# Optimization experiments

Hardware: AMD Instinct MI355X
Metric: run time of the kernel (lower is better)

## Reference

```python
import jax, jax.numpy as jnp
import numpy as np

B, T, N, E, I, H = 8, 168, 425, 2048, 128, 256
F1, F2 = 10, 32  # GCN hidden dims


def gcn(x, src, dst, w, W, b):
    """PyG-style GCNConv on one graph: x [N,f_in], src/dst [E], w [E]."""
    n = x.shape[0]
    h = x @ W  # [N, f_out]
    sl = jnp.arange(n, dtype=src.dtype)  # self loops, weight 1
    s = jnp.concatenate([src, sl])
    d = jnp.concatenate([dst, sl])
    ww = jnp.concatenate([w, jnp.ones((n,), w.dtype)])
    deg = jax.ops.segment_sum(ww, d, num_segments=n)
    dinv = jnp.where(deg > 0, jax.lax.rsqrt(jnp.maximum(deg, 1e-12)), 0.0)
    norm = dinv[s] * ww * dinv[d]
    return jax.ops.segment_sum(norm[:, None] * h[s], d, num_segments=n) + b


# vectorize over (batch, time)
_gcn_bt = jax.vmap(jax.vmap(gcn, in_axes=(0, 0, 0, 0, None, None)),
                   in_axes=(0, 0, 0, 0, None, None))


def lstm(xs, h0, c0, Wih, Whh, bih, bhh):
    """Single-layer torch LSTM (gate order i,f,g,o). xs [B,T,I] -> [B,T,H]."""
    def step(carry, x):
        h, c = carry
        g = x @ Wih.T + h @ Whh.T + bih + bhh  # [B,4H]
        i, f, gg, o = jnp.split(g, 4, axis=-1)
        c = jax.nn.sigmoid(f) * c + jax.nn.sigmoid(i) * jnp.tanh(gg)
        h = jax.nn.sigmoid(o) * jnp.tanh(c)
        return (h, c), h
    _, ys = jax.lax.scan(step, (h0, c0), xs.transpose(1, 0, 2))
    return ys.transpose(1, 0, 2)


def setup_inputs() -> dict:
    key = jax.random.key(0)
    ks = jax.random.split(key, 40)
    def p(i, shape, s=0.05):
        return jax.random.normal(ks[i], shape, jnp.float32) * s
    return {
        "node_feat": jax.random.uniform(ks[0], (B, T, N), jnp.float32),
        "edge_src": jax.random.randint(ks[1], (B, T, E), 0, N, jnp.int32),
        "edge_dst": jax.random.randint(ks[2], (B, T, E), 0, N, jnp.int32),
        "edge_weight": jax.random.uniform(ks[3], (B, T, E), jnp.float32),
        "infect": p(4, (B, T, 25), 1.0),
        "temp": p(5, (B, T, 13), 1.0),
        "h0": p(6, (1, B, H), 1.0),
        "c0": p(7, (1, B, H), 1.0),
        "Wg1": p(8, (1, F1)), "bg1": p(9, (F1,)),
        "Wg2": p(10, (F1, F2)), "bg2": p(11, (F2,)),
        "Wgfc": p(12, (N * F2, I)), "bgfc": p(13, (I,)),
        "Wi1": p(14, (25, 128)), "bi1": p(15, (128,)),
        "Wi2": p(16, (128, 128)), "bi2": p(17, (128,)),
        "Wi3": p(18, (128, 64)), "bi3": p(19, (64,)),
        "Wi4": p(20, (64, I)), "bi4": p(21, (I,)),
        "Wt1": p(22, (13, 64)), "bt1": p(23, (64,)),
        "Wt2": p(24, (64, I)), "bt2": p(25, (I,)),
        "Wcat": p(26, (3 * I, I)), "bcat": p(27, (I,)),
        "Wih": p(28, (4 * H, I)), "Whh": p(29, (4 * H, H)),
        "bih": p(30, (4 * H,)), "bhh": p(31, (4 * H,)),
        "Wfc": p(32, (H, 2 * N)), "bfc": p(33, (2 * N,)),
    }


def reference(node_feat, edge_src, edge_dst, edge_weight, infect, temp, h0, c0,
              Wg1, bg1, Wg2, bg2, Wgfc, bgfc,
              Wi1, bi1, Wi2, bi2, Wi3, bi3, Wi4, bi4,
              Wt1, bt1, Wt2, bt2, Wcat, bcat,
              Wih, Whh, bih, bhh, Wfc, bfc):
    r = jax.nn.relu
    # two-layer GCN per (batch, timestep) graph (deep_graph path)
    x1 = r(_gcn_bt(node_feat[..., None], edge_src, edge_dst, edge_weight, Wg1, bg1))
    x2 = r(_gcn_bt(x1, edge_src, edge_dst, edge_weight, Wg2, bg2))
    g = r(x2.reshape(B, T, N * F2) @ Wgfc + bgfc)  # graph branch [B,T,I]
    inf = r(infect @ Wi1 + bi1)
    inf = r(inf @ Wi2 + bi2)
    inf = r(inf @ Wi3 + bi3)
    inf = r(inf @ Wi4 + bi4)  # infect branch [B,T,I]
    tp = r(temp @ Wt1 + bt1)
    tp = r(tp @ Wt2 + bt2)  # temp branch [B,T,I]
    li = r(jnp.concatenate([g, inf, tp], axis=-1) @ Wcat + bcat)  # concat_fc path
    ys = r(lstm(li, h0[0], c0[0], Wih, Whh, bih, bhh))  # [B,T,H]
    out = r(ys[:, -1] @ Wfc + bfc)  # [B, 2N]
    # original splits by flattening the whole [B,2N] tensor
    flat = out.reshape(-1)
    user_pred = flat[: N * B].reshape(B, N)
    infect_pred = flat[N * B:].reshape(B, N)
    return user_pred, infect_pred
```

## Files before the change

### kernel.cpp

```cpp
#include <hip/hip_runtime.h>
#include <hip/hip_bf16.h>

#define BB 8
#define TT 168
#define NN 425
#define EE 2048
#define II 128
#define HH 256
#define F1 10
#define F2 32
#define BT (BB*TT)
#define K2 (NN*F2)
#define N2 (2*NN)

#define BREG_PW 46
#define BLDS_PW 18
#define BREG_N (8*BREG_PW*64)
#define BLDS_N (8*BLDS_PW*64)
#define LB 2

#define FR_TOTAL 444

typedef _Float16 h2 __attribute__((ext_vector_type(2)));
typedef _Float16 h8 __attribute__((ext_vector_type(8)));
typedef short bf16x8 __attribute__((ext_vector_type(8)));
typedef float f32x4 __attribute__((ext_vector_type(4)));

__device__ __forceinline__ float relu_(float x){ return fmaxf(x, 0.f); }
__device__ __forceinline__ float sigmoid_(float x){ return 1.f/(1.f + expf(-x)); }

#define MFMA16(ACC, AV, BV) \
    ACC = __builtin_amdgcn_mfma_f32_16x16x32_f16((AV), (BV), (ACC), 0, 0, 0)

__device__ __forceinline__ void ds_pk_add(h2* p, h2 v){
    unsigned a = (unsigned)(uintptr_t)p;
    asm volatile("ds_pk_add_f16 %0, %1" :: "v"(a), "v"(v) : "memory");
}

__device__ __forceinline__ h8 actld(const char* act, int K, int lane, int kc){
    int row = lane & 15;
    unsigned off = ((unsigned)(row*K + kc*32 + ((lane>>4)<<3))*2) ^ (unsigned)((row&7)<<4);
    return *(const h8*)(act + off);
}
__device__ __forceinline__ void actst(char* act, int K, int row, int col, _Float16 v){
    unsigned off = ((unsigned)(row*K + col)*2) ^ (unsigned)((row&7)<<4);
    *(_Float16*)(act + off) = v;
}

__global__ __launch_bounds__(256) void gcn_kernel(
    const float* __restrict__ nf, const int* __restrict__ esrc,
    const int* __restrict__ edst, const float* __restrict__ ew,
    const float* __restrict__ Wg1, const float* __restrict__ bg1,
    const float* __restrict__ Wg2, const float* __restrict__ bg2,
    __hip_bfloat16* __restrict__ x2g)
{
    __shared__ float xs[NN];
    __shared__ float dinv[NN];
    __shared__ float agg1[NN];
    __shared__ float nrm[EE];
    __shared__ __align__(16) float x1p[NN*12];
    __shared__ __align__(16) h2 agg2h[NN*8];
    __shared__ float wg1s[F1], bg1s[F1], wg2s[F1*F2], bg2s[F2];

    const int bt = blockIdx.x, tid = threadIdx.x;
    const long eb = (long)bt * EE;

    for (int v = tid; v < NN; v += 256) {
        xs[v] = nf[(long)bt*NN + v];
        dinv[v] = 1.0f;
        agg1[v] = 0.f;
    }
    for (int i = tid; i < NN*8; i += 256) agg2h[i] = (h2){(_Float16)0.f, (_Float16)0.f};
    if (tid < F1) { wg1s[tid] = Wg1[tid]; bg1s[tid] = bg1[tid]; }
    if (tid < F2) bg2s[tid] = bg2[tid];
    for (int i = tid; i < F1*F2; i += 256) wg2s[i] = Wg2[i];
    __syncthreads();

    for (int e = tid; e < EE; e += 256)
        atomicAdd(&dinv[edst[eb+e]], ew[eb+e]);
    __syncthreads();
    for (int v = tid; v < NN; v += 256) {
        float dg = dinv[v];
        dinv[v] = dg > 0.f ? 1.0f / sqrtf(fmaxf(dg, 1e-12f)) : 0.f;
    }
    __syncthreads();

    for (int e = tid; e < EE; e += 256) {
        int s = esrc[eb+e], d = edst[eb+e];
        float nm = dinv[s] * ew[eb+e] * dinv[d];
        nrm[e] = nm;
        atomicAdd(&agg1[d], nm * xs[s]);
    }
    __syncthreads();
    for (int v = tid; v < NN; v += 256) agg1[v] += dinv[v]*dinv[v]*xs[v];
    __syncthreads();
    for (int i = tid; i < NN*12; i += 256) {
        int v = i / 12, f = i - v*12;
        x1p[i] = (f < F1) ? relu_(agg1[v]*wg1s[f] + bg1s[f]) : 0.f;
    }
    __syncthreads();

    for (int e = tid; e < EE; e += 256) {
        int s = esrc[eb+e], d = edst[eb+e];
        float nm = nrm[e];
        float4 a0 = *(const float4*)&x1p[s*12];
        float4 a1 = *(const float4*)&x1p[s*12+4];
        float2 a2 = *(const float2*)&x1p[s*12+8];
        h2 p0; p0[0] = (_Float16)(nm*a0.x); p0[1] = (_Float16)(nm*a0.y);
        h2 p1; p1[0] = (_Float16)(nm*a0.z); p1[1] = (_Float16)(nm*a0.w);
        h2 p2; p2[0] = (_Float16)(nm*a1.x); p2[1] = (_Float16)(nm*a1.y);
        h2 p3; p3[0] = (_Float16)(nm*a1.z); p3[1] = (_Float16)(nm*a1.w);
        h2 p4; p4[0] = (_Float16)(nm*a2.x); p4[1] = (_Float16)(nm*a2.y);
        ds_pk_add(&agg2h[d*8+0], p0);
        ds_pk_add(&agg2h[d*8+1], p1);
        ds_pk_add(&agg2h[d*8+2], p2);
        ds_pk_add(&agg2h[d*8+3], p3);
        ds_pk_add(&agg2h[d*8+4], p4);
    }
    __syncthreads();

    {
        const int k = tid & 31;
        float wk[F1];
        #pragma unroll
        for (int f = 0; f < F1; ++f) wk[f] = wg2s[f*F2 + k];
        for (int i = tid; i < NN*F2; i += 256) {
            int v = i >> 5;
            float dv2 = dinv[v]*dinv[v];
            h8 r8 = *(const h8*)&agg2h[v*8];
            h2 r2 = agg2h[v*8+4];
            float4 a0 = *(const float4*)&x1p[v*12];
            float4 a1 = *(const float4*)&x1p[v*12+4];
            float2 a2 = *(const float2*)&x1p[v*12+8];
            float af[10];
            af[0]=(float)r8[0]+dv2*a0.x; af[1]=(float)r8[1]+dv2*a0.y;
            af[2]=(float)r8[2]+dv2*a0.z; af[3]=(float)r8[3]+dv2*a0.w;
            af[4]=(float)r8[4]+dv2*a1.x; af[5]=(float)r8[5]+dv2*a1.y;
            af[6]=(float)r8[6]+dv2*a1.z; af[7]=(float)r8[7]+dv2*a1.w;
            af[8]=(float)r2[0]+dv2*a2.x; af[9]=(float)r2[1]+dv2*a2.y;
            float o = bg2s[k];
            #pragma unroll
            for (int f = 0; f < F1; ++f) o += af[f]*wk[f];
            x2g[(long)bt*K2 + i] = __float2bfloat16(relu_(o));
        }
    }
}

__global__ __launch_bounds__(256) void packT_kernel(
    const float* __restrict__ W, __hip_bfloat16* __restrict__ out)
{
    __shared__ float tile[64][129];
    const int k0 = blockIdx.x * 64, tid = threadIdx.x;
    for (int i = tid; i < 64*128; i += 256) {
        int r = i >> 7, j = i & 127;
        tile[r][j] = (k0 + r < K2) ? W[(size_t)(k0+r)*II + j] : 0.f;
    }
    __syncthreads();
    for (int i = tid; i < 64*128; i += 256) {
        int j = i >> 6, r = i & 63;
        if (k0 + r < K2) out[(size_t)j*K2 + k0 + r] = __float2bfloat16(tile[r][j]);
    }
}

#define GBM 64
#define GBK 64
#define GCH 8
#define GST 27
__global__ __launch_bounds__(256) void gemm_kernel(
    const __hip_bfloat16* __restrict__ A, const __hip_bfloat16* __restrict__ Bt,
    float* __restrict__ C)
{
    __shared__ __align__(16) char As[2][GBM*GBK*2];
    __shared__ __align__(16) char Bs[2][II*GBK*2];
    const int tid = threadIdx.x;
    const int row0 = blockIdx.x * GBM;
    const int kbeg = blockIdx.y * (GST*GBK);
    const int wave = tid >> 6, lane = tid & 63;
    const int wm = wave >> 1, wn = wave & 1;
    const int l16 = lane & 15, lk = lane >> 4;
    const short* Aa = (const short*)A;
    const short* Bb = (const short*)Bt;

    const int ar = tid >> 2, ac = tid & 3;
    const int bc = tid >> 1, bh = (tid & 1) * 4;

    f32x4 acc[2][4];
    #pragma unroll
    for (int m = 0; m < 2; ++m)
        #pragma unroll
        for (int n = 0; n < 4; ++n) acc[m][n] = (f32x4){0.f,0.f,0.f,0.f};

    {
        #pragma unroll
        for (int j = 0; j < 2; ++j) {
            bf16x8 va = {0,0,0,0,0,0,0,0};
            int k = kbeg + ac*16 + j*8;
            if (k < K2) va = *(const bf16x8*)(Aa + (size_t)(row0+ar)*K2 + k);
            *(bf16x8*)(&As[0][0] + ((ar*128 + (ac*2+j)*16) ^ ((ar&7)<<4))) = va;
        }
        #pragma unroll
        for (int j = 0; j < 4; ++j) {
            bf16x8 vb = {0,0,0,0,0,0,0,0};
            int k = kbeg + (bh+j)*8;
            if (k < K2) vb = *(const bf16x8*)(Bb + (size_t)bc*K2 + k);
            *(bf16x8*)(&Bs[0][0] + ((bc*128 + (bh+j)*16) ^ ((bc&7)<<4))) = vb;
        }
    }
    __syncthreads();

    for (int s = 0; s < GST; ++s) {
        const int d = s & 1;
        bf16x8 pa[2], pb[4];
        #pragma unroll
        for (int j = 0; j < 2; ++j) pa[j] = (bf16x8){0,0,0,0,0,0,0,0};
        #pragma unroll
        for (int j = 0; j < 4; ++j) pb[j] = (bf16x8){0,0,0,0,0,0,0,0};
        if (s + 1 < GST) {
            int k0n = kbeg + (s+1)*GBK;
            #pragma unroll
            for (int j = 0; j < 2; ++j) {
                int k = k0n + ac*16 + j*8;
                if (k < K2) pa[j] = *(const bf16x8*)(Aa + (size_t)(row0+ar)*K2 + k);
            }
            #pragma unroll
            for (int j = 0; j < 4; ++j) {
                int k = k0n + (bh+j)*8;
                if (k < K2) pb[j] = *(const bf16x8*)(Bb + (size_t)bc*K2 + k);
            }
        }
        #pragma unroll
        for (int s2 = 0; s2 < 2; ++s2) {
            bf16x8 af[2], bf[4];
            #pragma unroll
            for (int m = 0; m < 2; ++m) {
                int row = wm*32 + m*16 + l16;
                af[m] = *(const bf16x8*)(&As[d][0] + ((row*128 + s2*64 + lk*16) ^ ((row&7)<<4)));
            }
            #pragma unroll
            for (int n = 0; n < 4; ++n) {
                int col = wn*64 + n*16 + l16;
                bf[n] = *(const bf16x8*)(&Bs[d][0] + ((col*128 + s2*64 + lk*16) ^ ((col&7)<<4)));
            }
            #pragma unroll
            for (int m = 0; m < 2; ++m)
                #pragma unroll
                for (int n = 0; n < 4; ++n)
                    acc[m][n] = __builtin_amdgcn_mfma_f32_16x16x32_bf16(af[m], bf[n], acc[m][n], 0, 0, 0);
        }
        if (s + 1 < GST) {
            #pragma unroll
            for (int j = 0; j < 2; ++j)
                *(bf16x8*)(&As[d^1][0] + ((ar*128 + (ac*2+j)*16) ^ ((ar&7)<<4))) = pa[j];
            #pragma unroll
            for (int j = 0; j < 4; ++j)
                *(bf16x8*)(&Bs[d^1][0] + ((bc*128 + (bh+j)*16) ^ ((bc&7)<<4))) = pb[j];
        }
        __syncthreads();
    }

    #pragma unroll
    for (int m = 0; m < 2; ++m)
        #pragma unroll
        for (int n = 0; n < 4; ++n)
            #pragma unroll
            for (int q = 0; q < 4; ++q)
                atomicAdd(&C[(size_t)(row0 + wm*32 + m*16 + lk*4 + q)*II + wn*64 + n*16 + l16],
                          acc[m][n][q]);
}

__global__ __launch_bounds__(64) void pack_frags_kernel(
    const float* __restrict__ Wi1, const float* __restrict__ Wi2,
    const float* __restrict__ Wi3, const float* __restrict__ Wi4,
    const float* __restrict__ Wt1, const float* __restrict__ Wt2,
    const float* __restrict__ Wcat, const float* __restrict__ Wih,
    h8* __restrict__ out)
{
    int f = blockIdx.x, l = threadIdx.x;
    const float* S; int sn, sk, K, KC, base;
    if      (f < 8)   { S=Wi1;  sn=1;   sk=128; K=25;  KC=1;  base=0;  }
    else if (f < 40)  { S=Wi2;  sn=1;   sk=128; K=128; KC=4;  base=8;  }
    else if (f < 56)  { S=Wi3;  sn=1;   sk=64;  K=128; KC=4;  base=40; }
    else if (f < 72)  { S=Wi4;  sn=1;   sk=128; K=64;  KC=2;  base=56; }
    else if (f < 76)  { S=Wt1;  sn=1;   sk=64;  K=13;  KC=1;  base=72; }
    else if (f < 92)  { S=Wt2;  sn=1;   sk=128; K=64;  KC=2;  base=76; }
    else if (f < 188) { S=Wcat; sn=1;   sk=128; K=384; KC=12; base=92; }
    else              { S=Wih;  sn=128; sk=1;   K=128; KC=4;  base=188;}
    int loc = f - base, nt = loc / KC, kc = loc % KC;
    int n = nt*16 + (l & 15);
    int k0 = kc*32 + ((l >> 4) << 3);
    h8 v;
    #pragma unroll
    for (int e = 0; e < 8; ++e) {
        int k = k0 + e;
        v[e] = (_Float16)((k < K) ? S[(size_t)n*sn + (size_t)k*sk] : 0.f);
    }
    out[(size_t)f*64 + l] = v;
}

__global__ __launch_bounds__(256) void blx_kernel(
    const float* __restrict__ infect, const float* __restrict__ temp,
    const float* __restrict__ g_pre, const float* __restrict__ bgfc,
    const float* __restrict__ bi1, const float* __restrict__ bi2,
    const float* __restrict__ bi3, const float* __restrict__ bi4,
    const float* __restrict__ bt1, const float* __restrict__ bt2,
    const float* __restrict__ bcat, const float* __restrict__ bih,
    const float* __restrict__ bhh, const h8* __restrict__ frags,
    float* __restrict__ xg4)
{
    __shared__ __align__(16) char CAT[16*384*2];
    __shared__ __align__(16) char S0[16*128*2];
    __shared__ __align__(16) char S1[16*128*2];
    __shared__ __align__(16) char LIb[16*128*2];
    __shared__ __align__(16) char XIN[16*32*2];
    __shared__ __align__(16) char XTt[16*32*2];
    __shared__ __align__(16) char XT1[16*64*2];

    const int tid = threadIdx.x, lane = tid & 63, w = tid >> 6;
    const int r0 = blockIdx.x * 16;
    const int c16 = lane & 15;
    const int rq = (lane >> 4) * 4;

    for (int i = tid; i < 16*32; i += 256) {
        int r = i >> 5, c = i & 31;
        actst(XIN, 32, r, c, (_Float16)((c < 25) ? infect[(size_t)(r0+r)*25 + c] : 0.f));
        actst(XTt, 32, r, c, (_Float16)((c < 13) ? temp[(size_t)(r0+r)*13 + c] : 0.f));
    }
    for (int i = tid; i < 16*128; i += 256) {
        int r = i >> 7, u = i & 127;
        actst(CAT, 384, r, u, (_Float16)relu_(g_pre[(size_t)(r0+r)*128 + u] + bgfc[u]));
    }
    __syncthreads();

    {
        h8 a = actld(XIN, 32, lane, 0);
        #pragma unroll
        for (int nt = w; nt < 8; nt += 4) {
            f32x4 acc = (f32x4){0.f,0.f,0.f,0.f};
            MFMA16(acc, a, frags[(size_t)(0 + nt)*64 + lane]);
            float bv = bi1[nt*16 + c16];
            #pragma unroll
            for (int q = 0; q < 4; ++q)
                actst(S0, 128, rq + q, nt*16 + c16, (_Float16)relu_(acc[q] + bv));
        }
        h8 at = actld(XTt, 32, lane, 0);
        {
            int nt = w;
            f32x4 acc = (f32x4){0.f,0.f,0.f,0.f};
            MFMA16(acc, at, frags[(size_t)(72 + nt)*64 + lane]);
            float bv = bt1[nt*16 + c16];
            #pragma unroll
            for (int q = 0; q < 4; ++q)
                actst(XT1, 64, rq + q, nt*16 + c16, (_Float16)relu_(acc[q] + bv));
        }
    }
    __syncthreads();

    {
        h8 a[4];
        #pragma unroll
        for (int kc = 0; kc < 4; ++kc) a[kc] = actld(S0, 128, lane, kc);
        #pragma unroll
        for (int nt = w; nt < 8; nt += 4) {
            f32x4 acc = (f32x4){0.f,0.f,0.f,0.f};
            #pragma unroll
            for (int kc = 0; kc < 4; ++kc)
                MFMA16(acc, a[kc], frags[(size_t)(8 + nt*4 + kc)*64 + lane]);
            float bv = bi2[nt*16 + c16];
            #pragma unroll
            for (int q = 0; q < 4; ++q)
                actst(S1, 128, rq + q, nt*16 + c16, (_Float16)relu_(acc[q] + bv));
        }
        h8 a2[2];
        #pragma unroll
        for (int kc = 0; kc < 2; ++kc) a2[kc] = actld(XT1, 64, lane, kc);
        #pragma unroll
        for (int nt = w; nt < 8; nt += 4) {
            f32x4 acc = (f32x4){0.f,0.f,0.f,0.f};
            #pragma unroll
            for (int kc = 0; kc < 2; ++kc)
                MFMA16(acc, a2[kc], frags[(size_t)(76 + nt*2 + kc)*64 + lane]);
            float bv = bt2[nt*16 + c16];
            #pragma unroll
            for (int q = 0; q < 4; ++q)
                actst(CAT, 384, rq + q, 256 + nt*16 + c16, (_Float16)relu_(acc[q] + bv));
        }
    }
    __syncthreads();

    {
        h8 a[4];
        #pragma unroll
        for (int kc = 0; kc < 4; ++kc) a[kc] = actld(S1, 128, lane, kc);
        int nt = w;
        f32x4 acc = (f32x4){0.f,0.f,0.f,0.f};
        #pragma unroll
        for (int kc = 0; kc < 4; ++kc)
            MFMA16(acc, a[kc], frags[(size_t)(40 + nt*4 + kc)*64 + lane]);
        float bv = bi3[nt*16 + c16];
        #pragma unroll
        for (int q = 0; q < 4; ++q)
            actst(XT1, 64, rq + q, nt*16 + c16, (_Float16)relu_(acc[q] + bv));
    }
    __syncthreads();

    {
        h8 a[2];
        #pragma unroll
        for (int kc = 0; kc < 2; ++kc) a[kc] = actld(XT1, 64, lane, kc);
        #pragma unroll
        for (int nt = w; nt < 8; nt += 4) {
            f32x4 acc = (f32x4){0.f,0.f,0.f,0.f};
            #pragma unroll
            for (int kc = 0; kc < 2; ++kc)
                MFMA16(acc, a[kc], frags[(size_t)(56 + nt*2 + kc)*64 + lane]);
            float bv = bi4[nt*16 + c16];
            #pragma unroll
            for (int q = 0; q < 4; ++q)
                actst(CAT, 384, rq + q, 128 + nt*16 + c16, (_Float16)relu_(acc[q] + bv));
        }
    }
    __syncthreads();

    {
        h8 a[12];
        #pragma unroll
        for (int kc = 0; kc < 12; ++kc) a[kc] = actld(CAT, 384, lane, kc);
        #pragma unroll
        for (int nt = w; nt < 8; nt += 4) {
            f32x4 acc = (f32x4){0.f,0.f,0.f,0.f};
            #pragma unroll
            for (int kc = 0; kc < 12; ++kc)
                MFMA16(acc, a[kc], frags[(size_t)(92 + nt*12 + kc)*64 + lane]);
            float bv = bcat[nt*16 + c16];
            #pragma unroll
            for (int q = 0; q < 4; ++q)
                actst(LIb, 128, rq + q, nt*16 + c16, (_Float16)relu_(acc[q] + bv));
        }
    }
    __syncthreads();

    {
        h8 a[4];
        #pragma unroll
        for (int kc = 0; kc < 4; ++kc) a[kc] = actld(LIb, 128, lane, kc);
        for (int nt = w; nt < 64; nt += 4) {
            f32x4 acc = (f32x4){0.f,0.f,0.f,0.f};
            #pragma unroll
            for (int kc = 0; kc < 4; ++kc)
                MFMA16(acc, a[kc], frags[(size_t)(188 + nt*4 + kc)*64 + lane]);
            int n = nt*16 + c16;
            int uu = n & 255, gg = n >> 8;
            float bv = bih[n] + bhh[n];
            #pragma unroll
            for (int q = 0; q < 4; ++q)
                xg4[(size_t)(r0 + rq + q)*1024 + uu*4 + gg] = acc[q] + bv;
        }
    }
}

__global__ __launch_bounds__(256) void pack_whh_kernel(
    const float* __restrict__ Whh, h8* __restrict__ bregp,
    h8* __restrict__ bldsp)
{
    int i = blockIdx.x*256 + threadIdx.x;
    int w, j, kc, lane;
    bool isreg = (i < BREG_N);
    if (isreg) {
        w = i / (BREG_PW*64); int r = i % (BREG_PW*64);
        int fidx = r >> 6; lane = r & 63;
        j  = (fidx < 42) ? fidx / 6 : 7;
        kc = (fidx < 42) ? fidx % 6 : fidx - 42;
    } else {
        int L = i - BREG_N;
        if (L >= BLDS_N) return;
        w = L / (BLDS_PW*64); int r = L % (BLDS_PW*64);
        int fidx = r >> 6; lane = r & 63;
        j  = (fidx < 14) ? (fidx >> 1) : 7;
        kc = (fidx < 14) ? 6 + (fidx & 1) : 4 + (fidx - 14);
    }
    int row = 128*w + 16*j + (lane & 15);
    int col = 32*kc + 8*(lane >> 4);
    h8 v;
    #pragma unroll
    for (int e = 0; e < 8; ++e) v[e] = (_Float16)Whh[(long)row*HH + col + e];
    if (isreg) bregp[i] = v; else bldsp[i - BREG_N] = v;
}

__attribute__((amdgpu_waves_per_eu(2, 2)))
__global__ __launch_bounds__(512) void lstm_kernel(
    const float* __restrict__ xg4, const h8* __restrict__ bregp,
    const h8* __restrict__ bldsp, const float* __restrict__ h0,
    const float* __restrict__ c0, float* __restrict__ hbuf)
{
    const int u = threadIdx.x;
    const int lane = u & 63;
    const int w = u >> 6;
    const int b0 = blockIdx.x * LB;
    const int bb = u >> 8, un = u & 255;
    const int Bg = b0 + bb;

    __shared__ __align__(16) h8 wlds[BLDS_N];
    __shared__ float gbuf[LB*1024];
    __shared__ __align__(16) char hbytes[2][LB*512];

    for (int i = u; i < BLDS_N; i += 512) wlds[i] = bldsp[i];

    h8 bfr[BREG_PW];
    {
        const h8* bp = bregp + (size_t)(w*BREG_PW)*64 + lane;
        #pragma unroll
        for (int m = 0; m < BREG_PW; ++m) bfr[m] = bp[(size_t)m*64];
    }

    float c = c0[Bg*HH + un];
    float h_last = 0.f;
    *(_Float16*)(&hbytes[0][0] + ((bb*512 + un*2) ^ (bb<<4))) = (_Float16)h0[Bg*HH + un];
    __syncthreads();

    const char* wbase = (const char*)wlds + w*(BLDS_PW*1024);
    const int br = lane & 1;
    const unsigned abase = (unsigned)((br*512 + ((lane>>4)<<3)*2) ^ (br<<4));
    const float4* xp = (const float4*)xg4;

    #pragma unroll 1
    for (int t = 0; t < TT; ++t) {
        const int cb = t & 1;
        float4 xv = xp[((size_t)Bg*TT + t)*256 + un];

        h8 a[8];
        #pragma unroll
        for (int kc = 0; kc < 8; ++kc)
            a[kc] = *(const h8*)(&hbytes[cb][0] + (abase ^ (unsigned)(kc*64)));

        f32x4 acc[8];
        #pragma unroll
        for (int j = 0; j < 8; ++j) acc[j] = (f32x4){0.f, 0.f, 0.f, 0.f};

        #pragma unroll
        for (int kc = 0; kc < 8; ++kc) {
            #pragma unroll
            for (int j = 0; j < 8; ++j) {
                h8 bv;
                if ((j < 7) ? (kc < 6) : (kc < 4)) {
                    bv = bfr[(j < 7) ? (j*6 + kc) : (42 + kc)];
                } else {
                    unsigned off = (unsigned)(((j < 7) ? (j*2 + kc - 6)
                                                       : (14 + kc - 4))*1024 + lane*16);
                    asm volatile("" : "+v"(off));
                    bv = *(const h8*)(wbase + off);
                }
                acc[j] = __builtin_amdgcn_mfma_f32_16x16x32_f16(a[kc], bv, acc[j], 0, 0, 0);
            }
        }

        if (lane < 16) {
            #pragma unroll
            for (int j = 0; j < 8; ++j) {
                int n = 128*w + j*16 + lane;
                gbuf[n]        = acc[j][0];
                gbuf[1024 + n] = acc[j][1];
            }
        }
        __syncthreads();

        {
            float gi = gbuf[bb*1024 + un]       + xv.x;
            float gf = gbuf[bb*1024 + 256 + un] + xv.y;
            float gg = gbuf[bb*1024 + 512 + un] + xv.z;
            float go = gbuf[bb*1024 + 768 + un] + xv.w;
            c = sigmoid_(gf)*c + sigmoid_(gi)*tanhf(gg);
            float h = sigmoid_(go)*tanhf(c);
            *(_Float16*)(&hbytes[cb^1][0] + ((bb*512 + un*2) ^ (bb<<4))) = (_Float16)h;
            h_last = h;
        }
        __syncthreads();
    }
    hbuf[Bg*HH + un] = h_last;
}

__global__ __launch_bounds__(256) void final_fc_kernel(
    const float* __restrict__ hbuf, const float* __restrict__ Wfc,
    const float* __restrict__ bfc, float* __restrict__ out)
{
    int idx = blockIdx.x*256 + threadIdx.x;
    if (idx >= BB*N2) return;
    int b = idx / N2, j = idx - b*N2;
    const float* h = hbuf + b*HH;
    float o = bfc[j];
    for (int k = 0; k < HH; ++k) o += fmaxf(h[k], 0.f) * Wfc[(long)k*N2 + j];
    out[idx] = relu_(o);
}

extern "C" void kernel_launch(void* const* d_in, const int* in_sizes, int n_in,
                              void* d_out, int out_size, void* d_ws, size_t ws_size,
                              hipStream_t stream) {
    const float* nf     = (const float*)d_in[0];
    const int*   esrc   = (const int*)d_in[1];
    const int*   edst   = (const int*)d_in[2];
    const float* ew     = (const float*)d_in[3];
    const float* infect = (const float*)d_in[4];
    const float* temp   = (const float*)d_in[5];
    const float* h0     = (const float*)d_in[6];
    const float* c0     = (const float*)d_in[7];
    const float* Wg1    = (const float*)d_in[8];
    const float* bg1    = (const float*)d_in[9];
    const float* Wg2    = (const float*)d_in[10];
    const float* bg2    = (const float*)d_in[11];
    const float* Wgfc   = (const float*)d_in[12];
    const float* bgfc   = (const float*)d_in[13];
    const float* Wi1    = (const float*)d_in[14];
    const float* bi1    = (const float*)d_in[15];
    const float* Wi2    = (const float*)d_in[16];
    const float* bi2    = (const float*)d_in[17];
    const float* Wi3    = (const float*)d_in[18];
    const float* bi3    = (const float*)d_in[19];
    const float* Wi4    = (const float*)d_in[20];
    const float* bi4    = (const float*)d_in[21];
    const float* Wt1    = (const float*)d_in[22];
    const float* bt1    = (const float*)d_in[23];
    const float* Wt2    = (const float*)d_in[24];
    const float* bt2    = (const float*)d_in[25];
    const float* Wcat   = (const float*)d_in[26];
    const float* bcat   = (const float*)d_in[27];
    const float* Wih    = (const float*)d_in[28];
    const float* Whh    = (const float*)d_in[29];
    const float* bih    = (const float*)d_in[30];
    const float* bhh    = (const float*)d_in[31];
    const float* Wfc    = (const float*)d_in[32];
    const float* bfc    = (const float*)d_in[33];

    char* ws = (char*)d_ws;
    size_t off = 0;
    __hip_bfloat16* x2g = (__hip_bfloat16*)(ws + off); off += (size_t)BT*K2*2;
    __hip_bfloat16* WgfcT = (__hip_bfloat16*)(ws + off); off += (size_t)II*K2*2;
    float* g_pre = (float*)(ws + off); off += (size_t)BT*II*4;
    float* xg4   = (float*)(ws + off); off += (size_t)BT*1024*4;
    float* hbuf  = (float*)(ws + off); off += (size_t)BB*HH*4;
    h8* bregp = (h8*)(ws + off); off += (size_t)BREG_N*16;
    h8* bldsp = (h8*)(ws + off); off += (size_t)BLDS_N*16;
    h8* frags = (h8*)(ws + off); off += (size_t)FR_TOTAL*64*16;

    hipMemsetAsync(g_pre, 0, (size_t)BT*II*4, stream);

    pack_whh_kernel<<<128, 256, 0, stream>>>(Whh, bregp, bldsp);
    pack_frags_kernel<<<FR_TOTAL, 64, 0, stream>>>(Wi1, Wi2, Wi3, Wi4, Wt1, Wt2,
                                                   Wcat, Wih, frags);
    packT_kernel<<<(K2 + 63)/64, 256, 0, stream>>>(Wgfc, WgfcT);
    gcn_kernel<<<BT, 256, 0, stream>>>(nf, esrc, edst, ew, Wg1, bg1, Wg2, bg2, x2g);
    gemm_kernel<<<dim3(BT/GBM, GCH), 256, 0, stream>>>(x2g, WgfcT, g_pre);
    blx_kernel<<<BT/16, 256, 0, stream>>>(infect, temp, g_pre, bgfc,
                                          bi1, bi2, bi3, bi4, bt1, bt2,
                                          bcat, bih, bhh, frags, xg4);
    lstm_kernel<<<BB/LB, 512, 0, stream>>>(xg4, bregp, bldsp, h0, c0, hbuf);
    final_fc_kernel<<<(BB*N2 + 255)/256, 256, 0, stream>>>(hbuf, Wfc, bfc, (float*)d_out);
}
```

Measured before the change: 586.4 us.

## Stream LSTM recurrent weights from global memory with double-buffered register prefetch

The LSTM kernel no longer keeps most of Whh resident in registers plus a slice in LDS. It packs all fragments into one global array and reloads them every timestep, double-buffering each k-chunk of eight fragments in registers while the MFMAs for the previous chunk run. This frees registers and LDS (the waves_per_eu attribute is dropped), but it adds about 512 KB of L2/global traffic per step on a latency-bound serial recurrence across 168 steps.

```diff
diff --git a/kernel.cpp b/kernel.cpp
--- a/kernel.cpp
+++ b/kernel.cpp
@@ -13,11 +13,8 @@
 #define K2 (NN*F2)
 #define N2 (2*NN)
 
-#define BREG_PW 46
-#define BLDS_PW 18
-#define BREG_N (8*BREG_PW*64)
-#define BLDS_N (8*BLDS_PW*64)
 #define LB 2
+#define FRW_N (8*64*64)
 
 #define FR_TOTAL 444
 
@@ -459,38 +456,24 @@
 }
 
 __global__ __launch_bounds__(256) void pack_whh_kernel(
-    const float* __restrict__ Whh, h8* __restrict__ bregp,
-    h8* __restrict__ bldsp)
+    const float* __restrict__ Whh, h8* __restrict__ fragsW)
 {
     int i = blockIdx.x*256 + threadIdx.x;
-    int w, j, kc, lane;
-    bool isreg = (i < BREG_N);
-    if (isreg) {
-        w = i / (BREG_PW*64); int r = i % (BREG_PW*64);
-        int fidx = r >> 6; lane = r & 63;
-        j  = (fidx < 42) ? fidx / 6 : 7;
-        kc = (fidx < 42) ? fidx % 6 : fidx - 42;
-    } else {
-        int L = i - BREG_N;
-        if (L >= BLDS_N) return;
-        w = L / (BLDS_PW*64); int r = L % (BLDS_PW*64);
-        int fidx = r >> 6; lane = r & 63;
-        j  = (fidx < 14) ? (fidx >> 1) : 7;
-        kc = (fidx < 14) ? 6 + (fidx & 1) : 4 + (fidx - 14);
-    }
+    int lane = i & 63;
+    int f = i >> 6;
+    int j = f & 7, kc = (f >> 3) & 7, w = f >> 6;
     int row = 128*w + 16*j + (lane & 15);
     int col = 32*kc + 8*(lane >> 4);
     h8 v;
     #pragma unroll
     for (int e = 0; e < 8; ++e) v[e] = (_Float16)Whh[(long)row*HH + col + e];
-    if (isreg) bregp[i] = v; else bldsp[i - BREG_N] = v;
-}
-
-__attribute__((amdgpu_waves_per_eu(2, 2)))
+    fragsW[i] = v;
+}
+
 __global__ __launch_bounds__(512) void lstm_kernel(
-    const float* __restrict__ xg4, const h8* __restrict__ bregp,
-    const h8* __restrict__ bldsp, const float* __restrict__ h0,
-    const float* __restrict__ c0, float* __restrict__ hbuf)
+    const float* __restrict__ xg4, const h8* __restrict__ fragsW,
+    const float* __restrict__ h0, const float* __restrict__ c0,
+    float* __restrict__ hbuf)
 {
     const int u = threadIdx.x;
     const int lane = u & 63;
@@ -499,28 +482,29 @@
     const int bb = u >> 8, un = u & 255;
     const int Bg = b0 + bb;
 
-    __shared__ __align__(16) h8 wlds[BLDS_N];
     __shared__ float gbuf[LB*1024];
     __shared__ __align__(16) char hbytes[2][LB*512];
-
-    for (int i = u; i < BLDS_N; i += 512) wlds[i] = bldsp[i];
-
-    h8 bfr[BREG_PW];
-    {
-        const h8* bp = bregp + (size_t)(w*BREG_PW)*64 + lane;
-        #pragma unroll
-        for (int m = 0; m < BREG_PW; ++m) bfr[m] = bp[(size_t)m*64];
-    }
 
     float c = c0[Bg*HH + un];
     float h_last = 0.f;
     *(_Float16*)(&hbytes[0][0] + ((bb*512 + un*2) ^ (bb<<4))) = (_Float16)h0[Bg*HH + un];
     __syncthreads();
 
-    const char* wbase = (const char*)wlds + w*(BLDS_PW*1024);
     const int br = lane & 1;
     const unsigned abase = (unsigned)((br*512 + ((lane>>4)<<3)*2) ^ (br<<4));
     const float4* xp = (const float4*)xg4;
+    const char* gwbase = (const char*)fragsW;
+    const unsigned tof = (unsigned)((w*64*64 + lane) * 16);
+
+    h8 wf[8], wg[8];
+    {
+        unsigned wo = tof;
+        asm volatile("" : "+v"(wo));
+        const char* gp = gwbase + wo;
+        #pragma unroll
+        for (int j = 0; j < 8; ++j)
+            wf[j] = *(const h8*)(gp + (unsigned)(j*1024));
+    }
 
     #pragma unroll 1
     for (int t = 0; t < TT; ++t) {
@@ -536,19 +520,30 @@
         #pragma unroll
         for (int j = 0; j < 8; ++j) acc[j] = (f32x4){0.f, 0.f, 0.f, 0.f};
 
+        unsigned wo = tof;
+        asm volatile("" : "+v"(wo));
+        const char* gp = gwbase + wo;
+
         #pragma unroll
         for (int kc = 0; kc < 8; ++kc) {
+            if (kc < 7) {
+                if ((kc & 1) == 0) {
+                    #pragma unroll
+                    for (int j = 0; j < 8; ++j)
+                        wg[j] = *(const h8*)(gp + (unsigned)(((kc+1)*8 + j)*1024));
+                } else {
+                    #pragma unroll
+                    for (int j = 0; j < 8; ++j)
+                        wf[j] = *(const h8*)(gp + (unsigned)(((kc+1)*8 + j)*1024));
+                }
+            } else {
+                #pragma unroll
+                for (int j = 0; j < 8; ++j)
+                    wf[j] = *(const h8*)(gp + (unsigned)(j*1024));
+            }
             #pragma unroll
             for (int j = 0; j < 8; ++j) {
-                h8 bv;
-                if ((j < 7) ? (kc < 6) : (kc < 4)) {
-                    bv = bfr[(j < 7) ? (j*6 + kc) : (42 + kc)];
-                } else {
-                    unsigned off = (unsigned)(((j < 7) ? (j*2 + kc - 6)
-                                                       : (14 + kc - 4))*1024 + lane*16);
-                    asm volatile("" : "+v"(off));
-                    bv = *(const h8*)(wbase + off);
-                }
+                h8 bv = ((kc & 1) == 0) ? wf[j] : wg[j];
                 acc[j] = __builtin_amdgcn_mfma_f32_16x16x32_f16(a[kc], bv, acc[j], 0, 0, 0);
             }
         }
@@ -636,13 +631,12 @@
     float* g_pre = (float*)(ws + off); off += (size_t)BT*II*4;
     float* xg4   = (float*)(ws + off); off += (size_t)BT*1024*4;
     float* hbuf  = (float*)(ws + off); off += (size_t)BB*HH*4;
-    h8* bregp = (h8*)(ws + off); off += (size_t)BREG_N*16;
-    h8* bldsp = (h8*)(ws + off); off += (size_t)BLDS_N*16;
-    h8* frags = (h8*)(ws + off); off += (size_t)FR_TOTAL*64*16;
+    h8* fragsW = (h8*)(ws + off); off += (size_t)FRW_N*16;
+    h8* frags  = (h8*)(ws + off); off += (size_t)FR_TOTAL*64*16;
 
     hipMemsetAsync(g_pre, 0, (size_t)BT*II*4, stream);
 
-    pack_whh_kernel<<<128, 256, 0, stream>>>(Whh, bregp, bldsp);
+    pack_whh_kernel<<<128, 256, 0, stream>>>(Whh, fragsW);
     pack_frags_kernel<<<FR_TOTAL, 64, 0, stream>>>(Wi1, Wi2, Wi3, Wi4, Wt1, Wt2,
                                                    Wcat, Wih, frags);
     packT_kernel<<<(K2 + 63)/64, 256, 0, stream>>>(Wgfc, WgfcT);
@@ -651,6 +645,6 @@
     blx_kernel<<<BT/16, 256, 0, stream>>>(infect, temp, g_pre, bgfc,
                                           bi1, bi2, bi3, bi4, bt1, bt2,
                                           bcat, bih, bhh, frags, xg4);
-    lstm_kernel<<<BB/LB, 512, 0, stream>>>(xg4, bregp, bldsp, h0, c0, hbuf);
+    lstm_kernel<<<BB/LB, 512, 0, stream>>>(xg4, fragsW, h0, c0, hbuf);
     final_fc_kernel<<<(BB*N2 + 255)/256, 256, 0, stream>>>(hbuf, Wfc, bfc, (float*)d_out);
 }
```

Measured after the change: 1.027 ms. 75.1% more time.
